# Kernel tuning notes

Hardware: AMD Instinct MI355X
Metric: run time of the kernel (lower is better)

The kernel has to match this reference:

```python
import jax, jax.numpy as jnp
import numpy as np

DIM = 32          # image/vq dim (ImageTransform3D default dim=32 == vq.layers[0].dim)
CODEBOOK = 1024   # number of codebook entries
TOTAL = 4194304   # flat weight-vector length (multiple of DIM)


def setup_inputs() -> dict:
    key = jax.random.key(0)
    k1, k2, k3 = jax.random.split(key, 3)
    weights = jax.random.normal(k1, (TOTAL,), dtype=jnp.float32)
    condition = jax.random.normal(k2, (1, DIM, TOTAL // DIM), dtype=jnp.float32)
    codebook = jax.random.normal(k3, (CODEBOOK, DIM), dtype=jnp.float32)
    return {"weights": weights, "condition": condition, "codebook": codebook}


def reference(weights, condition, codebook):
    # --- ImageTransform3D.forward: pad flat weights to a multiple of DIM, view (1, DIM, -1)
    pad = (-weights.shape[0]) % DIM  # static
    if pad:
        weights = jnp.concatenate([weights, jnp.zeros((pad,), weights.dtype)])
    img = weights.reshape(1, DIM, -1)
    # --- TokenTransform3D: subtract condition, flatten to tokens of size DIM
    x = (img - condition).reshape(-1, DIM)  # [N, DIM]
    # --- VectorQuantize (freeze_codebook, eval): nearest-neighbour lookup
    d = (
        jnp.sum(x * x, axis=-1, keepdims=True)
        - 2.0 * (x @ codebook.T)
        + jnp.sum(codebook * codebook, axis=-1)
    )
    indices = jnp.argmin(d, axis=-1)  # [N] int32
    return indices
```

## Files before the change

kernel.cpp:

```cpp
#include <hip/hip_runtime.h>

#define TOTAL     4194304
#define DIM       32
#define NTOK      (TOTAL / DIM)
#define NCODE     1024
#define CCODES    256
#define DELTA_EPS 2e-3f
#define FLAGBIT   0x40000000

typedef _Float16 half8   __attribute__((ext_vector_type(8)));
typedef float    floatx4 __attribute__((ext_vector_type(4)));

#define GLOAD_LDS16(g, l) \
    __builtin_amdgcn_global_load_lds((const __attribute__((address_space(1))) void*)(g), \
                                     (__attribute__((address_space(3))) void*)(l), 16, 0, 0)
#define GLOAD_LDS4(g, l) \
    __builtin_amdgcn_global_load_lds((const __attribute__((address_space(1))) void*)(g), \
                                     (__attribute__((address_space(3))) void*)(l), 4, 0, 0)

__global__ __launch_bounds__(64) void vq_prep(
    const float* __restrict__ cb, float* __restrict__ nhb,
    _Float16* __restrict__ Eh, _Float16* __restrict__ El)
{
    const int k = blockIdx.x * 64 + threadIdx.x;
    const float4* e4 = reinterpret_cast<const float4*>(cb) + (size_t)k * 8;
    float v[DIM];
    float4 t[8];
#pragma unroll
    for (int j = 0; j < 8; ++j) t[j] = e4[j];
#pragma unroll
    for (int j = 0; j < 8; ++j) {
        v[4 * j + 0] = t[j].x; v[4 * j + 1] = t[j].y;
        v[4 * j + 2] = t[j].z; v[4 * j + 3] = t[j].w;
    }
    float e2 = 0.0f;
#pragma unroll
    for (int i = 0; i < DIM; ++i) e2 = fmaf(v[i], v[i], e2);
    nhb[k] = -0.5f * e2;

    const int chunk = k >> 8, within = k & 255;
    const int step = within >> 4, l15 = within & 15;
#pragma unroll
    for (int l4 = 0; l4 < 4; ++l4) {
        half8 h, lo;
#pragma unroll
        for (int j = 0; j < 8; ++j) {
            float x = v[l4 * 8 + j];
            _Float16 hh = (_Float16)x;
            h[j]  = hh;
            lo[j] = (_Float16)(x - (float)hh);
        }
        const int slot = chunk * 1024 + step * 64 + l4 * 16 + l15;
        *reinterpret_cast<half8*>(Eh + (size_t)slot * 8) = h;
        *reinterpret_cast<half8*>(El + (size_t)slot * 8) = lo;
    }
}

__global__ __launch_bounds__(256) void vq_main(
    const float* __restrict__ w, const float* __restrict__ c,
    const float* __restrict__ nhb, const _Float16* __restrict__ Eh,
    const _Float16* __restrict__ El, const float* __restrict__ cb,
    int* __restrict__ out)
{
    __shared__ _Float16 sEh[1024 * 8];
    __shared__ _Float16 sEl[1024 * 8];
    __shared__ float    snh[CCODES];
    __shared__ int      sOut[128];

    const int tid  = threadIdx.x;
    const int lane = tid & 63;
    const int wid  = tid >> 6;
    const int tokw = blockIdx.x * 128 + wid * 32;
    const int l15  = lane & 15;
    const int l4   = lane >> 4;

    half8 xh[2], xl[2];
#pragma unroll
    for (int m = 0; m < 2; ++m) {
        const int token = tokw + m * 16 + l15;
        const float4* pw = reinterpret_cast<const float4*>(w + (size_t)token * DIM + l4 * 8);
        const float4* pc = reinterpret_cast<const float4*>(c + (size_t)token * DIM + l4 * 8);
        float4 a0 = pw[0], a1 = pw[1], b0 = pc[0], b1 = pc[1];
        float xs[8] = {a0.x - b0.x, a0.y - b0.y, a0.z - b0.z, a0.w - b0.w,
                       a1.x - b1.x, a1.y - b1.y, a1.z - b1.z, a1.w - b1.w};
#pragma unroll
        for (int j = 0; j < 8; ++j) {
            _Float16 h = (_Float16)xs[j];
            xh[m][j] = h;
            xl[m][j] = (_Float16)(xs[j] - (float)h);
        }
    }

    const float NEGINF = __uint_as_float(0xFF800000u);
    float best[8], second[8];
#pragma unroll
    for (int q = 0; q < 8; ++q) { best[q] = NEGINF; second[q] = NEGINF; }

    for (int ch = 0; ch < 4; ++ch) {
        if (ch) __syncthreads();
        {
            const _Float16* gh = Eh + (size_t)ch * 8192;
            const _Float16* gl = El + (size_t)ch * 8192;
#pragma unroll
            for (int r2 = 0; r2 < 4; ++r2) {
                const int slot = r2 * 256 + wid * 64;
                GLOAD_LDS16(gh + (size_t)(slot + lane) * 8, sEh + (size_t)slot * 8);
                GLOAD_LDS16(gl + (size_t)(slot + lane) * 8, sEl + (size_t)slot * 8);
            }
            GLOAD_LDS4(nhb + ch * CCODES + wid * 64 + lane, snh + wid * 64);
        }
        __syncthreads();

#pragma unroll
        for (int sp = 0; sp < 8; ++sp) {
            const int sA = 2 * sp, sB = 2 * sp + 1;
            const half8 ehA = *reinterpret_cast<const half8*>(sEh + (size_t)(sA * 64 + lane) * 8);
            const half8 elA = *reinterpret_cast<const half8*>(sEl + (size_t)(sA * 64 + lane) * 8);
            const half8 ehB = *reinterpret_cast<const half8*>(sEh + (size_t)(sB * 64 + lane) * 8);
            const half8 elB = *reinterpret_cast<const half8*>(sEl + (size_t)(sB * 64 + lane) * 8);
            const float nhA = snh[sA * 16 + l15];
            const float nhB = snh[sB * 16 + l15];
            const unsigned ixA = 1023u - (unsigned)(ch * CCODES + sA * 16 + l15);
            const unsigned ixB = ixA - 16u;
            const floatx4 nA = {nhA, nhA, nhA, nhA};
            const floatx4 nB = {nhB, nhB, nhB, nhB};
#pragma unroll
            for (int m = 0; m < 2; ++m) {
                floatx4 aA = __builtin_amdgcn_mfma_f32_16x16x32_f16(xh[m], ehA, nA, 0, 0, 0);
                aA = __builtin_amdgcn_mfma_f32_16x16x32_f16(xl[m], ehA, aA, 0, 0, 0);
                aA = __builtin_amdgcn_mfma_f32_16x16x32_f16(xh[m], elA, aA, 0, 0, 0);
                floatx4 aB = __builtin_amdgcn_mfma_f32_16x16x32_f16(xh[m], ehB, nB, 0, 0, 0);
                aB = __builtin_amdgcn_mfma_f32_16x16x32_f16(xl[m], ehB, aB, 0, 0, 0);
                aB = __builtin_amdgcn_mfma_f32_16x16x32_f16(xh[m], elB, aB, 0, 0, 0);
#pragma unroll
                for (int r = 0; r < 4; ++r) {
                    const int q = m * 4 + r;
                    float pA = __uint_as_float((__float_as_uint(aA[r]) & 0xFFFFFC00u) | ixA);
                    float pB = __uint_as_float((__float_as_uint(aB[r]) & 0xFFFFFC00u) | ixB);
                    second[q] = fmaxf(second[q], __builtin_amdgcn_fmed3f(pA, pB, best[q]));
                    best[q]   = fmaxf(fmaxf(best[q], pA), pB);
                }
            }
        }
    }

#pragma unroll
    for (int sh = 1; sh < 16; sh <<= 1) {
#pragma unroll
        for (int q = 0; q < 8; ++q) {
            float bB = __shfl_xor(best[q], sh);
            float sB = __shfl_xor(second[q], sh);
            second[q] = fmaxf(fmaxf(second[q], sB), fminf(best[q], bB));
            best[q]   = fmaxf(best[q], bB);
        }
    }

    if (l15 == 0) {
#pragma unroll
        for (int m = 0; m < 2; ++m) {
#pragma unroll
            for (int r = 0; r < 4; ++r) {
                const int q = m * 4 + r;
                unsigned ub = __float_as_uint(best[q]);
                unsigned us = __float_as_uint(second[q]);
                float bv = __uint_as_float(ub & 0xFFFFFC00u);
                float sv = __uint_as_float(us & 0xFFFFFC00u);
                int eb = (int)((ub >> 23) & 255u);
                int es = (int)((us >> 23) & 255u);
                int em = eb > es ? eb : es;
                em = em > 12 ? em : 12;
                float thr = __uint_as_float((unsigned)(em - 11) << 23) + DELTA_EPS;
                int k = 1023 - (int)(ub & 1023u);
                sOut[wid * 32 + m * 16 + l4 * 4 + r] = ((bv - sv) < thr) ? (k | FLAGBIT) : k;
            }
        }
    }

    int myval = 0;
    if (lane < 32) myval = sOut[wid * 32 + lane];
    unsigned long long mask = __ballot(lane < 32 && (myval & FLAGBIT));
    while (mask) {
        const int src = __ffsll(mask) - 1;
        mask &= mask - 1;
        const int token = tokw + src;

        float x[DIM];
#pragma unroll
        for (int j = 0; j < 8; ++j) {
            float4 aw = reinterpret_cast<const float4*>(w + (size_t)token * DIM)[j];
            float4 ac = reinterpret_cast<const float4*>(c + (size_t)token * DIM)[j];
            x[4 * j + 0] = aw.x - ac.x; x[4 * j + 1] = aw.y - ac.y;
            x[4 * j + 2] = aw.z - ac.z; x[4 * j + 3] = aw.w - ac.w;
        }
        float x2 = 0.f;
#pragma unroll
        for (int i = 0; i < DIM; ++i) x2 = fmaf(x[i], x[i], x2);

        float dmin = INFINITY;
        int   kbest = 0;
#pragma unroll 2
        for (int i = 0; i < 16; ++i) {
            const int k = lane + 64 * i;
            const float4* e4 = reinterpret_cast<const float4*>(cb) + (size_t)k * 8;
            float4 ev[8];
#pragma unroll
            for (int j = 0; j < 8; ++j) ev[j] = e4[j];
            float dot = 0.f;
#pragma unroll
            for (int j = 0; j < 8; ++j) {
                dot = fmaf(x[4 * j + 0], ev[j].x, dot);
                dot = fmaf(x[4 * j + 1], ev[j].y, dot);
                dot = fmaf(x[4 * j + 2], ev[j].z, dot);
                dot = fmaf(x[4 * j + 3], ev[j].w, dot);
            }
            float e2 = -2.0f * nhb[k];
            float dd = fmaf(-2.0f, dot, x2) + e2;
            if (dd < dmin) { dmin = dd; kbest = k; }
        }
#pragma unroll
        for (int sh = 1; sh < 64; sh <<= 1) {
            float dB = __shfl_xor(dmin, sh);
            int   iB = __shfl_xor(kbest, sh);
            bool take = (dB < dmin) || (dB == dmin && iB < kbest);
            dmin = take ? dB : dmin;
            kbest = take ? iB : kbest;
        }
        if (lane == src) myval = kbest;
    }
    if (lane < 32) out[tokw + lane] = myval;
}

extern "C" void kernel_launch(void* const* d_in, const int* in_sizes, int n_in,
                              void* d_out, int out_size, void* d_ws, size_t ws_size,
                              hipStream_t stream) {
    const float* w  = (const float*)d_in[0];
    const float* c  = (const float*)d_in[1];
    const float* cb = (const float*)d_in[2];
    int* out = (int*)d_out;

    char* wsb = (char*)d_ws;
    float*    nhb = (float*)wsb;
    _Float16* Eh  = (_Float16*)(wsb + 4096);
    _Float16* El  = (_Float16*)(wsb + 4096 + 65536);

    vq_prep<<<NCODE / 64, 64, 0, stream>>>(cb, nhb, Eh, El);
    vq_main<<<NTOK / 128, 256, 0, stream>>>(w, c, nhb, Eh, El, cb, out);
}
```

Before: 55.64 us.

## Split each block's 128 tokens across 8 waves of 16 tokens

```diff
diff --git a/kernel.cpp b/kernel.cpp
--- a/kernel.cpp
+++ b/kernel.cpp
@@ -56,7 +56,7 @@
     }
 }
 
-__global__ __launch_bounds__(256) void vq_main(
+__global__ __launch_bounds__(512, 8) void vq_main(
     const float* __restrict__ w, const float* __restrict__ c,
     const float* __restrict__ nhb, const _Float16* __restrict__ Eh,
     const _Float16* __restrict__ El, const float* __restrict__ cb,
@@ -70,14 +70,13 @@
     const int tid  = threadIdx.x;
     const int lane = tid & 63;
     const int wid  = tid >> 6;
-    const int tokw = blockIdx.x * 128 + wid * 32;
+    const int tokw = blockIdx.x * 128 + wid * 16;
     const int l15  = lane & 15;
     const int l4   = lane >> 4;
 
-    half8 xh[2], xl[2];
-#pragma unroll
-    for (int m = 0; m < 2; ++m) {
-        const int token = tokw + m * 16 + l15;
+    half8 xh, xl;
+    {
+        const int token = tokw + l15;
         const float4* pw = reinterpret_cast<const float4*>(w + (size_t)token * DIM + l4 * 8);
         const float4* pc = reinterpret_cast<const float4*>(c + (size_t)token * DIM + l4 * 8);
         float4 a0 = pw[0], a1 = pw[1], b0 = pc[0], b1 = pc[1];
@@ -86,15 +85,15 @@
 #pragma unroll
         for (int j = 0; j < 8; ++j) {
             _Float16 h = (_Float16)xs[j];
-            xh[m][j] = h;
-            xl[m][j] = (_Float16)(xs[j] - (float)h);
+            xh[j] = h;
+            xl[j] = (_Float16)(xs[j] - (float)h);
         }
     }
 
     const float NEGINF = __uint_as_float(0xFF800000u);
-    float best[8], second[8];
-#pragma unroll
-    for (int q = 0; q < 8; ++q) { best[q] = NEGINF; second[q] = NEGINF; }
+    float best[4], second[4];
+#pragma unroll
+    for (int q = 0; q < 4; ++q) { best[q] = NEGINF; second[q] = NEGINF; }
 
     for (int ch = 0; ch < 4; ++ch) {
         if (ch) __syncthreads();
@@ -102,12 +101,12 @@
             const _Float16* gh = Eh + (size_t)ch * 8192;
             const _Float16* gl = El + (size_t)ch * 8192;
 #pragma unroll
-            for (int r2 = 0; r2 < 4; ++r2) {
-                const int slot = r2 * 256 + wid * 64;
+            for (int r2 = 0; r2 < 2; ++r2) {
+                const int slot = r2 * 512 + wid * 64;
                 GLOAD_LDS16(gh + (size_t)(slot + lane) * 8, sEh + (size_t)slot * 8);
                 GLOAD_LDS16(gl + (size_t)(slot + lane) * 8, sEl + (size_t)slot * 8);
             }
-            GLOAD_LDS4(nhb + ch * CCODES + wid * 64 + lane, snh + wid * 64);
+            if (wid < 4) GLOAD_LDS4(nhb + ch * CCODES + wid * 64 + lane, snh + wid * 64);
         }
         __syncthreads();
 
@@ -124,22 +123,18 @@
             const unsigned ixB = ixA - 16u;
             const floatx4 nA = {nhA, nhA, nhA, nhA};
             const floatx4 nB = {nhB, nhB, nhB, nhB};
-#pragma unroll
-            for (int m = 0; m < 2; ++m) {
-                floatx4 aA = __builtin_amdgcn_mfma_f32_16x16x32_f16(xh[m], ehA, nA, 0, 0, 0);
-                aA = __builtin_amdgcn_mfma_f32_16x16x32_f16(xl[m], ehA, aA, 0, 0, 0);
-                aA = __builtin_amdgcn_mfma_f32_16x16x32_f16(xh[m], elA, aA, 0, 0, 0);
-                floatx4 aB = __builtin_amdgcn_mfma_f32_16x16x32_f16(xh[m], ehB, nB, 0, 0, 0);
-                aB = __builtin_amdgcn_mfma_f32_16x16x32_f16(xl[m], ehB, aB, 0, 0, 0);
-                aB = __builtin_amdgcn_mfma_f32_16x16x32_f16(xh[m], elB, aB, 0, 0, 0);
-#pragma unroll
-                for (int r = 0; r < 4; ++r) {
-                    const int q = m * 4 + r;
-                    float pA = __uint_as_float((__float_as_uint(aA[r]) & 0xFFFFFC00u) | ixA);
-                    float pB = __uint_as_float((__float_as_uint(aB[r]) & 0xFFFFFC00u) | ixB);
-                    second[q] = fmaxf(second[q], __builtin_amdgcn_fmed3f(pA, pB, best[q]));
-                    best[q]   = fmaxf(fmaxf(best[q], pA), pB);
-                }
+            floatx4 aA = __builtin_amdgcn_mfma_f32_16x16x32_f16(xh, ehA, nA, 0, 0, 0);
+            aA = __builtin_amdgcn_mfma_f32_16x16x32_f16(xl, ehA, aA, 0, 0, 0);
+            aA = __builtin_amdgcn_mfma_f32_16x16x32_f16(xh, elA, aA, 0, 0, 0);
+            floatx4 aB = __builtin_amdgcn_mfma_f32_16x16x32_f16(xh, ehB, nB, 0, 0, 0);
+            aB = __builtin_amdgcn_mfma_f32_16x16x32_f16(xl, ehB, aB, 0, 0, 0);
+            aB = __builtin_amdgcn_mfma_f32_16x16x32_f16(xh, elB, aB, 0, 0, 0);
+#pragma unroll
+            for (int r = 0; r < 4; ++r) {
+                float pA = __uint_as_float((__float_as_uint(aA[r]) & 0xFFFFFC00u) | ixA);
+                float pB = __uint_as_float((__float_as_uint(aB[r]) & 0xFFFFFC00u) | ixB);
+                second[r] = fmaxf(second[r], __builtin_amdgcn_fmed3f(pA, pB, best[r]));
+                best[r]   = fmaxf(fmaxf(best[r], pA), pB);
             }
         }
     }
@@ -147,7 +142,7 @@
 #pragma unroll
     for (int sh = 1; sh < 16; sh <<= 1) {
 #pragma unroll
-        for (int q = 0; q < 8; ++q) {
+        for (int q = 0; q < 4; ++q) {
             float bB = __shfl_xor(best[q], sh);
             float sB = __shfl_xor(second[q], sh);
             second[q] = fmaxf(fmaxf(second[q], sB), fminf(best[q], bB));
@@ -157,28 +152,24 @@
 
     if (l15 == 0) {
 #pragma unroll
-        for (int m = 0; m < 2; ++m) {
-#pragma unroll
-            for (int r = 0; r < 4; ++r) {
-                const int q = m * 4 + r;
-                unsigned ub = __float_as_uint(best[q]);
-                unsigned us = __float_as_uint(second[q]);
-                float bv = __uint_as_float(ub & 0xFFFFFC00u);
-                float sv = __uint_as_float(us & 0xFFFFFC00u);
-                int eb = (int)((ub >> 23) & 255u);
-                int es = (int)((us >> 23) & 255u);
-                int em = eb > es ? eb : es;
-                em = em > 12 ? em : 12;
-                float thr = __uint_as_float((unsigned)(em - 11) << 23) + DELTA_EPS;
-                int k = 1023 - (int)(ub & 1023u);
-                sOut[wid * 32 + m * 16 + l4 * 4 + r] = ((bv - sv) < thr) ? (k | FLAGBIT) : k;
-            }
+        for (int r = 0; r < 4; ++r) {
+            unsigned ub = __float_as_uint(best[r]);
+            unsigned us = __float_as_uint(second[r]);
+            float bv = __uint_as_float(ub & 0xFFFFFC00u);
+            float sv = __uint_as_float(us & 0xFFFFFC00u);
+            int eb = (int)((ub >> 23) & 255u);
+            int es = (int)((us >> 23) & 255u);
+            int em = eb > es ? eb : es;
+            em = em > 12 ? em : 12;
+            float thr = __uint_as_float((unsigned)(em - 11) << 23) + DELTA_EPS;
+            int k = 1023 - (int)(ub & 1023u);
+            sOut[wid * 16 + l4 * 4 + r] = ((bv - sv) < thr) ? (k | FLAGBIT) : k;
         }
     }
 
     int myval = 0;
-    if (lane < 32) myval = sOut[wid * 32 + lane];
-    unsigned long long mask = __ballot(lane < 32 && (myval & FLAGBIT));
+    if (lane < 16) myval = sOut[wid * 16 + lane];
+    unsigned long long mask = __ballot(lane < 16 && (myval & FLAGBIT));
     while (mask) {
         const int src = __ffsll(mask) - 1;
         mask &= mask - 1;
@@ -227,7 +218,7 @@
         }
         if (lane == src) myval = kbest;
     }
-    if (lane < 32) out[tokw + lane] = myval;
+    if (lane < 16) out[tokw + lane] = myval;
 }
 
 extern "C" void kernel_launch(void* const* d_in, const int* in_sizes, int n_in,
@@ -244,5 +235,5 @@
     _Float16* El  = (_Float16*)(wsb + 4096 + 65536);
 
     vq_prep<<<NCODE / 64, 64, 0, stream>>>(cb, nhb, Eh, El);
-    vq_main<<<NTOK / 128, 256, 0, stream>>>(w, c, nhb, Eh, El, cb, out);
+    vq_main<<<NTOK / 128, 512, 0, stream>>>(w, c, nhb, Eh, El, cb, out);
 }
```

Result: slower. 60.60 us (+8.9%).
